# Kernel tuning notes

Measured on AMD Instinct MI355X. Metric: run time of the kernel, lower is better.

The kernel has to match this reference:

```python
import jax, jax.numpy as jnp
import numpy as np
from jax import lax

DIM = 4096
N_HEADS = 32
N_KV_HEADS = 8
HEAD_DIM = DIM // N_HEADS  # 128
N_REP = N_HEADS // N_KV_HEADS  # 4
B, S = 1, 2048
ROPE_THETA = 10000.0
NEG_INF = -1e9


def setup_inputs() -> dict:
    key = jax.random.key(0)
    ks = jax.random.split(key, 6)
    scale = 1.0 / np.sqrt(DIM)
    x = jax.random.normal(ks[0], (B, S, DIM), dtype=jnp.float32)
    wq = jax.random.normal(ks[1], (DIM, DIM), dtype=jnp.float32) * scale
    wk = jax.random.normal(ks[2], (N_KV_HEADS * HEAD_DIM, DIM), dtype=jnp.float32) * scale
    wv = jax.random.normal(ks[3], (N_KV_HEADS * HEAD_DIM, DIM), dtype=jnp.float32) * scale
    wo = jax.random.normal(ks[4], (DIM, DIM), dtype=jnp.float32) * scale
    # Llama rotary frequencies: freqs_cis[t, i] = exp(i * t * theta^(-2i/d))
    inv_freq = 1.0 / (ROPE_THETA ** (np.arange(0, HEAD_DIM, 2, dtype=np.float32) / HEAD_DIM))
    angles = np.outer(np.arange(S, dtype=np.float32), inv_freq)  # [S, HEAD_DIM//2]
    freqs_cos = jnp.asarray(np.cos(angles), dtype=jnp.float32)
    freqs_sin = jnp.asarray(np.sin(angles), dtype=jnp.float32)
    cache_k = jnp.zeros((B, S, N_KV_HEADS, HEAD_DIM), dtype=jnp.float32)
    cache_v = jnp.zeros((B, S, N_KV_HEADS, HEAD_DIM), dtype=jnp.float32)
    # causal mask added to scores (broadcasts over [B, H, S, S])
    mask = jnp.where(np.triu(np.ones((S, S), dtype=bool), k=1), NEG_INF, 0.0).astype(jnp.float32)
    return {"x": x, "wq": wq, "wk": wk, "wv": wv, "wo": wo,
            "freqs_cos": freqs_cos, "freqs_sin": freqs_sin,
            "cache_k": cache_k, "cache_v": cache_v, "mask": mask,
            "start_pos": 0}


def _apply_rotary(t, cos, sin):
    # t: [B, S, H, HEAD_DIM]; cos/sin: [S, HEAD_DIM//2]
    b, s, h, d = t.shape
    tr = t.reshape(b, s, h, d // 2, 2)
    a, bb = tr[..., 0], tr[..., 1]  # real / imag of consecutive pairs
    c = cos[None, :, None, :]
    sn = sin[None, :, None, :]
    out_r = a * c - bb * sn
    out_i = a * sn + bb * c
    return jnp.stack([out_r, out_i], axis=-1).reshape(b, s, h, d)


def reference(x, wq, wk, wv, wo, freqs_cos, freqs_sin, cache_k, cache_v, mask, start_pos):
    bsz, seqlen, _ = x.shape
    xq = jnp.einsum('bsd,od->bso', x, wq).reshape(bsz, seqlen, N_HEADS, HEAD_DIM)
    xk = jnp.einsum('bsd,od->bso', x, wk).reshape(bsz, seqlen, N_KV_HEADS, HEAD_DIM)
    xv = jnp.einsum('bsd,od->bso', x, wv).reshape(bsz, seqlen, N_KV_HEADS, HEAD_DIM)
    xq = _apply_rotary(xq, freqs_cos, freqs_sin)
    xk = _apply_rotary(xk, freqs_cos, freqs_sin)
    # KV-cache append
    cache_k = lax.dynamic_update_slice(cache_k, xk, (0, start_pos, 0, 0))
    cache_v = lax.dynamic_update_slice(cache_v, xv, (0, start_pos, 0, 0))
    kv_len = start_pos + seqlen
    keys = cache_k[:, :kv_len]    # [B, KVLEN, KV, HD]
    values = cache_v[:, :kv_len]
    # GQA: repeat_interleave over kv heads
    keys = jnp.repeat(keys, N_REP, axis=2)      # [B, KVLEN, H, HD]
    values = jnp.repeat(values, N_REP, axis=2)
    q = xq.transpose(0, 2, 1, 3)       # [B, H, S, HD]
    k = keys.transpose(0, 2, 1, 3)     # [B, H, KVLEN, HD]
    v = values.transpose(0, 2, 1, 3)
    scores = jnp.einsum('bhqd,bhkd->bhqk', q, k) / np.sqrt(HEAD_DIM)
    scores = scores + mask[None, None, :, :]
    probs = jax.nn.softmax(scores.astype(jnp.float32), axis=-1).astype(q.dtype)
    out = jnp.einsum('bhqk,bhkd->bhqd', probs, v)
    out = out.transpose(0, 2, 1, 3).reshape(bsz, seqlen, -1)
    return jnp.einsum('bso,do->bsd', out, wo)
```

## Files before the change

### kernel.cpp

```cpp
#include <hip/hip_runtime.h>
#include <hip/hip_bf16.h>

typedef unsigned short u16;
typedef unsigned int u32;
typedef __bf16 bf16x8 __attribute__((ext_vector_type(8)));
typedef float f32x4 __attribute__((ext_vector_type(4)));
typedef u32 u32x4 __attribute__((ext_vector_type(4)));

#define QKV_LD 6144
#define KOFF 4096
#define VOFF 5120
#define HD 128
#define DIM 4096

__device__ __forceinline__ u16 f2bf(float f) {
  union { __hip_bfloat16 h; u16 u; } c;
  c.h = __float2bfloat16(f);
  return c.u;
}
__device__ __forceinline__ float bf2f(u16 u) {
  union { u16 u; __hip_bfloat16 h; } c;
  c.u = u;
  return __bfloat162float(c.h);
}

typedef __attribute__((address_space(1))) const u32 gas_u32;
typedef __attribute__((address_space(3))) u32 las_u32;
__device__ __forceinline__ void async16(const u16* g, u16* l) {
  __builtin_amdgcn_global_load_lds((gas_u32*)g, (las_u32*)l, 16, 0, 0);
}

__device__ __forceinline__ void store_out(u16* p, float v) { *p = f2bf(v); }
__device__ __forceinline__ void store_out(float* p, float v) { *p = v; }

__global__ __launch_bounds__(256) void cvt_kernel(const float* __restrict__ src,
                                                  u16* __restrict__ dst, int n8) {
  int i = blockIdx.x * 256 + threadIdx.x;
  if (i >= n8) return;
  const f32x4* s4 = (const f32x4*)src;
  f32x4 a = s4[2 * i], b = s4[2 * i + 1];
  u32x4 o;
  o[0] = (u32)f2bf(a[0]) | ((u32)f2bf(a[1]) << 16);
  o[1] = (u32)f2bf(a[2]) | ((u32)f2bf(a[3]) << 16);
  o[2] = (u32)f2bf(b[0]) | ((u32)f2bf(b[1]) << 16);
  o[3] = (u32)f2bf(b[2]) | ((u32)f2bf(b[3]) << 16);
  ((u32x4*)dst)[i] = o;
}

template <typename OutT>
__global__ __launch_bounds__(256, 2) void gemm_nt(const u16* __restrict__ A,
                                                  const u16* __restrict__ B,
                                                  OutT* __restrict__ C, int N, int K) {
  __shared__ u16 As[128 * 32];
  __shared__ u16 Bs[128 * 32];
  const int tid = threadIdx.x;
  const int wave = tid >> 6;
  const int lane = tid & 63;
  const int quad = lane >> 4;
  const int l16 = lane & 15;
  const int bm = blockIdx.y;
  const int bn = blockIdx.x;
  const int wm = (wave >> 1) * 64;
  const int wn = (wave & 1) * 64;

  f32x4 acc[4][4];
#pragma unroll
  for (int i = 0; i < 4; ++i)
#pragma unroll
    for (int j = 0; j < 4; ++j) {
      f32x4 z = {0.f, 0.f, 0.f, 0.f};
      acc[i][j] = z;
    }

  const int srow0 = wave * 32 + (lane >> 2);
  const int scol = (((lane & 3) ^ ((lane >> 2) & 3)) * 8);
  u16* ldsA0 = &As[(wave * 2 + 0) * 512];
  u16* ldsA1 = &As[(wave * 2 + 1) * 512];
  u16* ldsB0 = &Bs[(wave * 2 + 0) * 512];
  u16* ldsB1 = &Bs[(wave * 2 + 1) * 512];
  const u16* Ag0 = A + (size_t)(bm * 128 + srow0) * K + scol;
  const u16* Ag1 = A + (size_t)(bm * 128 + srow0 + 16) * K + scol;
  const u16* Bg0 = B + (size_t)(bn * 128 + srow0) * K + scol;
  const u16* Bg1 = B + (size_t)(bn * 128 + srow0 + 16) * K + scol;

  int aoff[4], boff[4];
#pragma unroll
  for (int mi = 0; mi < 4; ++mi)
    aoff[mi] = (wm + mi * 16 + l16) * 32 + ((quad ^ (l16 & 3)) * 8);
#pragma unroll
  for (int ni = 0; ni < 4; ++ni)
    boff[ni] = (wn + ni * 16 + l16) * 32 + ((quad ^ (l16 & 3)) * 8);

  for (int k0 = 0; k0 < K; k0 += 32) {
    __syncthreads();
    async16(Ag0 + k0, ldsA0);
    async16(Ag1 + k0, ldsA1);
    async16(Bg0 + k0, ldsB0);
    async16(Bg1 + k0, ldsB1);
    __syncthreads();
    bf16x8 af[4], bb[4];
#pragma unroll
    for (int mi = 0; mi < 4; ++mi) af[mi] = *(const bf16x8*)&As[aoff[mi]];
#pragma unroll
    for (int ni = 0; ni < 4; ++ni) bb[ni] = *(const bf16x8*)&Bs[boff[ni]];
#pragma unroll
    for (int mi = 0; mi < 4; ++mi)
#pragma unroll
      for (int ni = 0; ni < 4; ++ni)
        acc[mi][ni] = __builtin_amdgcn_mfma_f32_16x16x32_bf16(af[mi], bb[ni], acc[mi][ni], 0, 0, 0);
  }

#pragma unroll
  for (int mi = 0; mi < 4; ++mi) {
    int row = bm * 128 + wm + mi * 16 + quad * 4;
#pragma unroll
    for (int ni = 0; ni < 4; ++ni) {
      int col = bn * 128 + wn + ni * 16 + l16;
#pragma unroll
      for (int r = 0; r < 4; ++r)
        store_out(&C[(size_t)(row + r) * N + col], acc[mi][ni][r]);
    }
  }
}

#define BAR8 __builtin_amdgcn_s_barrier()
#define LGKM0                                                     \
  do {                                                            \
    asm volatile("s_waitcnt lgkmcnt(0)" ::: "memory");            \
    __builtin_amdgcn_sched_barrier(0);                            \
  } while (0)
#define VMC(n)                                                    \
  do {                                                            \
    asm volatile("s_waitcnt vmcnt(" #n ")" ::: "memory");         \
    __builtin_amdgcn_sched_barrier(0);                            \
  } while (0)

#define LDA8(buf, half, arr)                                                     \
  _Pragma("unroll") for (int mi = 0; mi < 4; ++mi) {                             \
    const int r_ = wm * 64 + mi * 16 + l16;                                      \
    const u16* p_ = &lds[buf][half][r_ * 64];                                    \
    _Pragma("unroll") for (int ks = 0; ks < 2; ++ks)                             \
      arr[mi][ks] = *(const bf16x8*)(p_ + (((ks * 4 + quad) ^ (r_ & 7)) << 3));  \
  }

#define LDB8(buf, half, arr)                                                     \
  _Pragma("unroll") for (int ni = 0; ni < 2; ++ni) {                             \
    const int r_ = wn * 32 + ni * 16 + l16;                                      \
    const u16* p_ = &lds[buf][2 + (half)][r_ * 64];                              \
    _Pragma("unroll") for (int ks = 0; ks < 2; ++ks)                             \
      arr[ni][ks] = *(const bf16x8*)(p_ + (((ks * 4 + quad) ^ (r_ & 7)) << 3));  \
  }

#define MMA8(qm, qn, af, bf)                                                       \
  __builtin_amdgcn_s_setprio(1);                                                   \
  _Pragma("unroll") for (int mi = 0; mi < 4; ++mi)                                 \
  _Pragma("unroll") for (int ni = 0; ni < 2; ++ni)                                 \
  _Pragma("unroll") for (int ks = 0; ks < 2; ++ks)                                 \
    acc[(qm) * 4 + mi][(qn) * 2 + ni] = __builtin_amdgcn_mfma_f32_16x16x32_bf16(   \
        af[mi][ks], bf[ni][ks], acc[(qm) * 4 + mi][(qn) * 2 + ni], 0, 0, 0);       \
  __builtin_amdgcn_s_setprio(0);

template <typename OutT>
__global__ __launch_bounds__(512, 2) void gemm_nt8(const u16* __restrict__ A,
                                                   const u16* __restrict__ B,
                                                   OutT* __restrict__ C,
                                                   int N, int K, int MT) {
  __shared__ u16 lds[2][4][128 * 64];
  const int tid = threadIdx.x;
  const int wave = tid >> 6;
  const int lane = tid & 63;
  const int quad = lane >> 4;
  const int l16 = lane & 15;
  const int wm = wave >> 2;
  const int wn = wave & 3;

  const int nwg = gridDim.x;
  const int bid = blockIdx.x;
  const int qq = nwg >> 3, rr8 = nwg & 7, xcd = bid & 7, off = bid >> 3;
  const int wg = (xcd < rr8 ? xcd * (qq + 1) : rr8 * (qq + 1) + (xcd - rr8) * qq) + off;
  const int bm = wg % MT;
  const int bn = wg / MT;

  const int NIT = K >> 7;

  const int srow = (wave << 3) + (lane >> 3);
  const int sgran = (lane & 7) ^ ((lane >> 3) & 7);
  const u16* Abase = A + (size_t)(bm * 256 + srow) * K + sgran * 8;
  const u16* Bbase = B + (size_t)(bn * 256 + srow) * K + sgran * 8;

  auto stage = [&](const u16* base, int h, int kt, u16* slot) {
    const u16* g = base + (size_t)(h * 128) * K + kt * 64;
    u16* s = slot + wave * (8 * 64);
    async16(g, s);
    async16(g + (size_t)64 * K, s + 64 * 64);
  };

  f32x4 acc[8][4];
#pragma unroll
  for (int i = 0; i < 8; ++i)
#pragma unroll
    for (int j = 0; j < 4; ++j) {
      f32x4 z = {0.f, 0.f, 0.f, 0.f};
      acc[i][j] = z;
    }

  stage(Abase, 0, 0, &lds[0][0][0]);
  stage(Bbase, 0, 0, &lds[0][2][0]);
  stage(Bbase, 1, 0, &lds[0][3][0]);
  stage(Abase, 1, 0, &lds[0][1][0]);
  stage(Abase, 0, 1, &lds[1][0][0]);
  stage(Bbase, 0, 1, &lds[1][2][0]);
  stage(Bbase, 1, 1, &lds[1][3][0]);
  VMC(6);
  BAR8;

  bf16x8 a0[4][2], a1[4][2], b0[2][2], b1[2][2];
  for (int it = 0; it < NIT; ++it) {
    const int t2 = 2 * it + 2, t3 = 2 * it + 3;
    const bool more = (it + 1 < NIT);

    LDA8(0, 0, a0);
    LDB8(0, 0, b0);
    stage(Abase, 1, 2 * it + 1, &lds[1][1][0]);
    BAR8; LGKM0;
    MMA8(0, 0, a0, b0);
    BAR8;
    LDB8(0, 1, b1);
    if (more) stage(Abase, 0, t2, &lds[0][0][0]);
    BAR8; LGKM0;
    MMA8(0, 1, a0, b1);
    BAR8;
    LDA8(0, 1, a1);
    if (more) stage(Bbase, 0, t2, &lds[0][2][0]);
    BAR8; LGKM0;
    MMA8(1, 1, a1, b1);
    BAR8;
    if (more) stage(Bbase, 1, t2, &lds[0][3][0]);
    BAR8; LGKM0;
    MMA8(1, 0, a1, b0);
    if (more) { VMC(6); } else { VMC(0); }
    BAR8;
    LDA8(1, 0, a0);
    LDB8(1, 0, b0);
    if (more) stage(Abase, 1, t2, &lds[0][1][0]);
    BAR8; LGKM0;
    MMA8(0, 0, a0, b0);
    BAR8;
    LDB8(1, 1, b1);
    if (more) stage(Abase, 0, t3, &lds[1][0][0]);
    BAR8; LGKM0;
    MMA8(0, 1, a0, b1);
    BAR8;
    LDA8(1, 1, a1);
    if (more) stage(Bbase, 0, t3, &lds[1][2][0]);
    BAR8; LGKM0;
    MMA8(1, 1, a1, b1);
    BAR8;
    if (more) stage(Bbase, 1, t3, &lds[1][3][0]);
    BAR8; LGKM0;
    MMA8(1, 0, a1, b0);
    if (more) { VMC(6); } else { VMC(0); }
    BAR8;
  }

#pragma unroll
  for (int qm = 0; qm < 2; ++qm)
#pragma unroll
    for (int mi = 0; mi < 4; ++mi) {
      int row = bm * 256 + qm * 128 + wm * 64 + mi * 16 + quad * 4;
#pragma unroll
      for (int qn = 0; qn < 2; ++qn)
#pragma unroll
        for (int ni = 0; ni < 2; ++ni) {
          int col = bn * 256 + qn * 128 + wn * 32 + ni * 16 + l16;
#pragma unroll
          for (int r = 0; r < 4; ++r)
            store_out(&C[(size_t)(row + r) * N + col], acc[qm * 4 + mi][qn * 2 + ni][r]);
        }
    }
}

__global__ __launch_bounds__(256) void rope_kernel(u16* qkv, const float* __restrict__ fcos,
                                                   const float* __restrict__ fsin) {
  int idx = blockIdx.x * 256 + threadIdx.x;
  int row, colbase, fi;
  if (idx < 2048 * 2048) {
    row = idx >> 11;
    int pi = idx & 2047;
    fi = pi & 63;
    colbase = (pi >> 6) * 128 + fi * 2;
  } else {
    int j = idx - 2048 * 2048;
    row = j >> 9;
    int pj = j & 511;
    fi = pj & 63;
    colbase = KOFF + (pj >> 6) * 128 + fi * 2;
  }
  float c = fcos[row * 64 + fi], s = fsin[row * 64 + fi];
  u32* p = (u32*)(qkv + (size_t)row * QKV_LD + colbase);
  u32 v = *p;
  float a = bf2f((u16)(v & 0xffffu));
  float b = bf2f((u16)(v >> 16));
  float xr = a * c - b * s;
  float xi = a * s + b * c;
  *p = (u32)f2bf(xr) | ((u32)f2bf(xi) << 16);
}

__global__ __launch_bounds__(256) void vtrans_kernel(const u16* __restrict__ qkv,
                                                     u16* __restrict__ vt) {
  __shared__ u16 Ls[64 * 72];
  const int tid = threadIdx.x;
  const int st = blockIdx.x, dt = blockIdx.y, kvh = blockIdx.z;
#pragma unroll
  for (int t = 0; t < 2; ++t) {
    int g = t * 256 + tid;
    int s = g >> 3, c = g & 7;
    u32x4 v = *(const u32x4*)(qkv + (size_t)(st * 64 + s) * QKV_LD + VOFF + kvh * HD + dt * 64 + c * 8);
    *(u32x4*)&Ls[s * 72 + c * 8] = v;
  }
  __syncthreads();
#pragma unroll
  for (int t = 0; t < 2; ++t) {
    int g = t * 256 + tid;
    int d = g >> 3, c2 = g & 7;
    u32x4 o;
#pragma unroll
    for (int j = 0; j < 4; ++j) {
      u16 lo = Ls[(c2 * 8 + 2 * j) * 72 + d];
      u16 hi = Ls[(c2 * 8 + 2 * j + 1) * 72 + d];
      o[j] = (u32)lo | ((u32)hi << 16);
    }
    *(u32x4*)(vt + (size_t)(kvh * HD + dt * 64 + d) * 2048 + st * 64 + c2 * 8) = o;
  }
}

__global__ __launch_bounds__(256, 2) void flash_kernel(const u16* __restrict__ qkv,
                                                       const u16* __restrict__ vt,
                                                       u16* __restrict__ attnb) {
  __shared__ u16 Kl[2][64 * 128];
  __shared__ u16 VtL[2][128 * 64];
  __shared__ u16 Pl[4][16 * 72];
  const int tid = threadIdx.x;
  const int wave = tid >> 6;
  const int lane = tid & 63;
  const int quad = lane >> 4;
  const int l16 = lane & 15;
  const int lid = blockIdx.x;
  const int h = lid & 31;
  const int z = lid >> 5;
  const int qt = (z < 8) ? z : 23 - z;
  const int kvh = h >> 2;
  const float scale = 0.08838834764831845f;
  const int nkt = 2 * qt + 2;

  const int krow_l = (lane >> 4);
  const int kcol_l = (lane & 15);
  const int vd_l = (lane >> 3);
  const int vc = (lane & 7) ^ ((lane >> 3) & 7);

  const u16* kbase = qkv + (size_t)KOFF + kvh * HD;
  const u16* vbase = vt + (size_t)kvh * HD * 2048;

  bf16x8 qf[2][4];
#pragma unroll
  for (int mi = 0; mi < 2; ++mi) {
    const u16* qp = qkv + (size_t)(qt * 128 + wave * 32 + mi * 16 + l16) * QKV_LD + h * HD + quad * 8;
#pragma unroll
    for (int ks = 0; ks < 4; ++ks) qf[mi][ks] = *(const bf16x8*)(qp + ks * 32);
  }

  f32x4 o[2][8];
#pragma unroll
  for (int mi = 0; mi < 2; ++mi)
#pragma unroll
    for (int i = 0; i < 8; ++i) { f32x4 zz = {0.f, 0.f, 0.f, 0.f}; o[mi][i] = zz; }
  float lacc[2] = {0.f, 0.f};

#pragma unroll
  for (int t = 0; t < 4; ++t) {
    int i = wave * 4 + t;
    int row = i * 4 + krow_l;
    int c = kcol_l ^ (row & 15);
    async16(kbase + (size_t)row * QKV_LD + c * 8, &Kl[0][i * 512]);
  }
#pragma unroll
  for (int t = 0; t < 4; ++t) {
    int i = wave * 4 + t;
    int d = i * 8 + vd_l;
    async16(vbase + (size_t)d * 2048 + vc * 8, &VtL[0][i * 512]);
  }

  for (int kt = 0; kt < nkt; ++kt) {
    const int cur = kt & 1;
    __syncthreads();

    f32x4 s4[2][4];
#pragma unroll
    for (int mi = 0; mi < 2; ++mi)
#pragma unroll
      for (int nb = 0; nb < 4; ++nb) { f32x4 zz = {0.f, 0.f, 0.f, 0.f}; s4[mi][nb] = zz; }
#pragma unroll
    for (int nb = 0; nb < 4; ++nb) {
#pragma unroll
      for (int ks = 0; ks < 4; ++ks) {
        int rr = nb * 16 + l16;
        int cc = ((ks * 4 + quad) ^ l16) * 8;
        bf16x8 kf = *(const bf16x8*)&Kl[cur][rr * 128 + cc];
        s4[0][nb] = __builtin_amdgcn_mfma_f32_16x16x32_bf16(qf[0][ks], kf, s4[0][nb], 0, 0, 0);
        s4[1][nb] = __builtin_amdgcn_mfma_f32_16x16x32_bf16(qf[1][ks], kf, s4[1][nb], 0, 0, 0);
      }
    }

    bf16x8 vb[16];
#pragma unroll
    for (int db = 0; db < 8; ++db) {
      int dd = db * 16 + l16;
#pragma unroll
      for (int ks2 = 0; ks2 < 2; ++ks2) {
        int c = (ks2 * 4 + quad) ^ (dd & 7);
        vb[db * 2 + ks2] = *(const bf16x8*)&VtL[cur][dd * 64 + c * 8];
      }
    }

    float p[2][4][4];
    const bool diag = (kt >= 2 * qt);
    if (diag) {
#pragma unroll
      for (int mi = 0; mi < 2; ++mi)
#pragma unroll
        for (int nb = 0; nb < 4; ++nb) {
          int col = kt * 64 + nb * 16 + l16;
#pragma unroll
          for (int r = 0; r < 4; ++r) {
            int row = qt * 128 + wave * 32 + mi * 16 + quad * 4 + r;
            p[mi][nb][r] = (col > row) ? 0.f : __expf(s4[mi][nb][r] * scale);
          }
        }
    } else {
#pragma unroll
      for (int mi = 0; mi < 2; ++mi)
#pragma unroll
        for (int nb = 0; nb < 4; ++nb)
#pragma unroll
          for (int r = 0; r < 4; ++r)
            p[mi][nb][r] = __expf(s4[mi][nb][r] * scale);
    }

    bf16x8 pa[2][2];
#pragma unroll
    for (int mi = 0; mi < 2; ++mi) {
#pragma unroll
      for (int nb = 0; nb < 4; ++nb)
#pragma unroll
        for (int r = 0; r < 4; ++r)
          Pl[wave][(quad * 4 + r) * 72 + nb * 16 + l16] = f2bf(p[mi][nb][r]);
      __asm__ __volatile__("s_waitcnt lgkmcnt(0)" ::: "memory");
#pragma unroll
      for (int ks2 = 0; ks2 < 2; ++ks2)
        pa[mi][ks2] = *(const bf16x8*)&Pl[wave][l16 * 72 + ks2 * 32 + quad * 8];
    }

#pragma unroll
    for (int mi = 0; mi < 2; ++mi) {
      float sm = 0.f;
#pragma unroll
      for (int ks2 = 0; ks2 < 2; ++ks2)
#pragma unroll
        for (int j = 0; j < 8; ++j) sm += (float)pa[mi][ks2][j];
      sm += __shfl_xor(sm, 16);
      sm += __shfl_xor(sm, 32);
      lacc[mi] += sm;
    }

    if (kt + 1 < nkt) {
      const u16* kb = kbase + (size_t)(kt + 1) * 64 * QKV_LD;
      const u16* vb2 = vbase + (kt + 1) * 64;
#pragma unroll
      for (int t = 0; t < 4; ++t) {
        int i = wave * 4 + t;
        int row = i * 4 + krow_l;
        int c = kcol_l ^ (row & 15);
        async16(kb + (size_t)row * QKV_LD + c * 8, &Kl[1 - cur][i * 512]);
      }
#pragma unroll
      for (int t = 0; t < 4; ++t) {
        int i = wave * 4 + t;
        int d = i * 8 + vd_l;
        async16(vb2 + (size_t)d * 2048 + vc * 8, &VtL[1 - cur][i * 512]);
      }
    }

#pragma unroll
    for (int mi = 0; mi < 2; ++mi)
#pragma unroll
      for (int db = 0; db < 8; ++db)
#pragma unroll
        for (int ks2 = 0; ks2 < 2; ++ks2)
          o[mi][db] = __builtin_amdgcn_mfma_f32_16x16x32_bf16(pa[mi][ks2], vb[db * 2 + ks2], o[mi][db], 0, 0, 0);
  }

  float* lsh = (float*)&Pl[wave][0];
  if (quad == 0) {
    lsh[l16] = lacc[0];
    lsh[16 + l16] = lacc[1];
  }
  __asm__ __volatile__("s_waitcnt lgkmcnt(0)" ::: "memory");
  __builtin_amdgcn_wave_barrier();
  f32x4 inv[2];
#pragma unroll
  for (int mi = 0; mi < 2; ++mi) {
    f32x4 lv = *(const f32x4*)&lsh[mi * 16 + quad * 4];
#pragma unroll
    for (int r = 0; r < 4; ++r) inv[mi][r] = 1.f / lv[r];
  }
#pragma unroll
  for (int mi = 0; mi < 2; ++mi)
#pragma unroll
    for (int db = 0; db < 8; ++db)
#pragma unroll
      for (int r = 0; r < 4; ++r) {
        int row = qt * 128 + wave * 32 + mi * 16 + quad * 4 + r;
        int col = h * HD + db * 16 + l16;
        attnb[(size_t)row * DIM + col] = f2bf(o[mi][db][r] * inv[mi][r]);
      }
}

extern "C" void kernel_launch(void* const* d_in, const int* in_sizes, int n_in,
                              void* d_out, int out_size, void* d_ws, size_t ws_size,
                              hipStream_t stream) {
  (void)in_sizes; (void)n_in; (void)out_size; (void)ws_size;
  const float* x    = (const float*)d_in[0];
  const float* wq   = (const float*)d_in[1];
  const float* wk   = (const float*)d_in[2];
  const float* wv   = (const float*)d_in[3];
  const float* wo   = (const float*)d_in[4];
  const float* fcos = (const float*)d_in[5];
  const float* fsin = (const float*)d_in[6];
  float* out = (float*)d_out;

  char* ws = (char*)d_ws;
  u16* xb    = (u16*)(ws);
  u16* wqkvb = (u16*)(ws + (size_t)16777216);
  u16* wob   = (u16*)(ws + (size_t)67108864);
  u16* qkv   = (u16*)(ws + (size_t)100663296);
  u16* attnb = (u16*)(ws + (size_t)125829120);
  u16* vtb   = (u16*)(ws);

  cvt_kernel<<<4096, 256, 0, stream>>>(x, xb, 1048576);
  cvt_kernel<<<8192, 256, 0, stream>>>(wq, wqkvb, 2097152);
  cvt_kernel<<<2048, 256, 0, stream>>>(wk, wqkvb + 16777216, 524288);
  cvt_kernel<<<2048, 256, 0, stream>>>(wv, wqkvb + 20971520, 524288);
  cvt_kernel<<<8192, 256, 0, stream>>>(wo, wob, 2097152);

  gemm_nt8<u16><<<dim3(192), 512, 0, stream>>>(xb, wqkvb, qkv, 6144, 4096, 8);
  vtrans_kernel<<<dim3(32, 2, 8), 256, 0, stream>>>(qkv, vtb);
  rope_kernel<<<20480, 256, 0, stream>>>(qkv, fcos, fsin);
  flash_kernel<<<512, 256, 0, stream>>>(qkv, vtb, attnb);
  gemm_nt<float><<<dim3(32, 16), 256, 0, stream>>>(attnb, wob, out, 4096, 4096);
}
```

Measured before the change: 550.5 us.

## Replace output projection GEMM with pipelined 128x256 8-wave kernel

The output projection, previously a simple 128x128 tile GEMM with two barriers per 32-wide K step, now runs on a new 512-thread kernel. It uses 128x256 tiles, double-buffered 64-wide K staging with async loads interleaved between MFMA phases, and XCD-aware block remapping over 256 workgroups. The goal is to hide global load latency and make better use of the MFMA units for the 4096x4096x2048 GEMM. The wait macros also lose their sched_barrier, which gives the compiler more scheduling freedom but could reorder code around the waits, and this applies to the existing gemm_nt8 as well.

After: 535.2 us. 1.03x faster.

```diff
diff --git a/kernel.cpp b/kernel.cpp
--- a/kernel.cpp
+++ b/kernel.cpp
@@ -47,93 +47,9 @@
   ((u32x4*)dst)[i] = o;
 }
 
-template <typename OutT>
-__global__ __launch_bounds__(256, 2) void gemm_nt(const u16* __restrict__ A,
-                                                  const u16* __restrict__ B,
-                                                  OutT* __restrict__ C, int N, int K) {
-  __shared__ u16 As[128 * 32];
-  __shared__ u16 Bs[128 * 32];
-  const int tid = threadIdx.x;
-  const int wave = tid >> 6;
-  const int lane = tid & 63;
-  const int quad = lane >> 4;
-  const int l16 = lane & 15;
-  const int bm = blockIdx.y;
-  const int bn = blockIdx.x;
-  const int wm = (wave >> 1) * 64;
-  const int wn = (wave & 1) * 64;
-
-  f32x4 acc[4][4];
-#pragma unroll
-  for (int i = 0; i < 4; ++i)
-#pragma unroll
-    for (int j = 0; j < 4; ++j) {
-      f32x4 z = {0.f, 0.f, 0.f, 0.f};
-      acc[i][j] = z;
-    }
-
-  const int srow0 = wave * 32 + (lane >> 2);
-  const int scol = (((lane & 3) ^ ((lane >> 2) & 3)) * 8);
-  u16* ldsA0 = &As[(wave * 2 + 0) * 512];
-  u16* ldsA1 = &As[(wave * 2 + 1) * 512];
-  u16* ldsB0 = &Bs[(wave * 2 + 0) * 512];
-  u16* ldsB1 = &Bs[(wave * 2 + 1) * 512];
-  const u16* Ag0 = A + (size_t)(bm * 128 + srow0) * K + scol;
-  const u16* Ag1 = A + (size_t)(bm * 128 + srow0 + 16) * K + scol;
-  const u16* Bg0 = B + (size_t)(bn * 128 + srow0) * K + scol;
-  const u16* Bg1 = B + (size_t)(bn * 128 + srow0 + 16) * K + scol;
-
-  int aoff[4], boff[4];
-#pragma unroll
-  for (int mi = 0; mi < 4; ++mi)
-    aoff[mi] = (wm + mi * 16 + l16) * 32 + ((quad ^ (l16 & 3)) * 8);
-#pragma unroll
-  for (int ni = 0; ni < 4; ++ni)
-    boff[ni] = (wn + ni * 16 + l16) * 32 + ((quad ^ (l16 & 3)) * 8);
-
-  for (int k0 = 0; k0 < K; k0 += 32) {
-    __syncthreads();
-    async16(Ag0 + k0, ldsA0);
-    async16(Ag1 + k0, ldsA1);
-    async16(Bg0 + k0, ldsB0);
-    async16(Bg1 + k0, ldsB1);
-    __syncthreads();
-    bf16x8 af[4], bb[4];
-#pragma unroll
-    for (int mi = 0; mi < 4; ++mi) af[mi] = *(const bf16x8*)&As[aoff[mi]];
-#pragma unroll
-    for (int ni = 0; ni < 4; ++ni) bb[ni] = *(const bf16x8*)&Bs[boff[ni]];
-#pragma unroll
-    for (int mi = 0; mi < 4; ++mi)
-#pragma unroll
-      for (int ni = 0; ni < 4; ++ni)
-        acc[mi][ni] = __builtin_amdgcn_mfma_f32_16x16x32_bf16(af[mi], bb[ni], acc[mi][ni], 0, 0, 0);
-  }
-
-#pragma unroll
-  for (int mi = 0; mi < 4; ++mi) {
-    int row = bm * 128 + wm + mi * 16 + quad * 4;
-#pragma unroll
-    for (int ni = 0; ni < 4; ++ni) {
-      int col = bn * 128 + wn + ni * 16 + l16;
-#pragma unroll
-      for (int r = 0; r < 4; ++r)
-        store_out(&C[(size_t)(row + r) * N + col], acc[mi][ni][r]);
-    }
-  }
-}
-
 #define BAR8 __builtin_amdgcn_s_barrier()
-#define LGKM0                                                     \
-  do {                                                            \
-    asm volatile("s_waitcnt lgkmcnt(0)" ::: "memory");            \
-    __builtin_amdgcn_sched_barrier(0);                            \
-  } while (0)
-#define VMC(n)                                                    \
-  do {                                                            \
-    asm volatile("s_waitcnt vmcnt(" #n ")" ::: "memory");         \
-    __builtin_amdgcn_sched_barrier(0);                            \
-  } while (0)
+#define LGKM0 asm volatile("s_waitcnt lgkmcnt(0)" ::: "memory")
+#define VMC(n) asm volatile("s_waitcnt vmcnt(" #n ")" ::: "memory")
 
 #define LDA8(buf, half, arr)                                                     \
   _Pragma("unroll") for (int mi = 0; mi < 4; ++mi) {                             \
@@ -276,6 +192,149 @@
 #pragma unroll
           for (int r = 0; r < 4; ++r)
             store_out(&C[(size_t)(row + r) * N + col], acc[qm * 4 + mi][qn * 2 + ni][r]);
+        }
+    }
+}
+
+#define LDAW(buf, arr)                                                               \
+  _Pragma("unroll") for (int qm_ = 0; qm_ < 2; ++qm_)                                \
+  _Pragma("unroll") for (int mi = 0; mi < 2; ++mi) {                                 \
+    const int r_ = qm_ * 64 + wm * 32 + mi * 16 + l16;                               \
+    const u16* p_ = &lds[buf][0][r_ * 64];                                           \
+    _Pragma("unroll") for (int ks = 0; ks < 2; ++ks)                                 \
+      arr[qm_][mi][ks] = *(const bf16x8*)(p_ + (((ks * 4 + quad) ^ (r_ & 7)) << 3)); \
+  }
+
+#define LDBW(buf, h, arr)                                                        \
+  _Pragma("unroll") for (int ni = 0; ni < 2; ++ni) {                             \
+    const int r_ = wn * 32 + ni * 16 + l16;                                      \
+    const u16* p_ = &lds[buf][1 + (h)][r_ * 64];                                 \
+    _Pragma("unroll") for (int ks = 0; ks < 2; ++ks)                             \
+      arr[ni][ks] = *(const bf16x8*)(p_ + (((ks * 4 + quad) ^ (r_ & 7)) << 3));  \
+  }
+
+#define MMAW(qm, qn, af, bf)                                                       \
+  __builtin_amdgcn_s_setprio(1);                                                   \
+  _Pragma("unroll") for (int mi = 0; mi < 2; ++mi)                                 \
+  _Pragma("unroll") for (int ni = 0; ni < 2; ++ni)                                 \
+  _Pragma("unroll") for (int ks = 0; ks < 2; ++ks)                                 \
+    acc[(qm) * 2 + mi][(qn) * 2 + ni] = __builtin_amdgcn_mfma_f32_16x16x32_bf16(   \
+        af[qm][mi][ks], bf[ni][ks], acc[(qm) * 2 + mi][(qn) * 2 + ni], 0, 0, 0);   \
+  __builtin_amdgcn_s_setprio(0);
+
+template <typename OutT>
+__global__ __launch_bounds__(512, 2) void gemm_nt8w(const u16* __restrict__ A,
+                                                    const u16* __restrict__ B,
+                                                    OutT* __restrict__ C,
+                                                    int N, int K, int MT) {
+  __shared__ u16 lds[2][3][128 * 64];
+  const int tid = threadIdx.x;
+  const int wave = tid >> 6;
+  const int lane = tid & 63;
+  const int quad = lane >> 4;
+  const int l16 = lane & 15;
+  const int wm = wave >> 2;
+  const int wn = wave & 3;
+
+  const int nwg = gridDim.x;
+  const int bid = blockIdx.x;
+  const int qq = nwg >> 3, rr8 = nwg & 7, xcd = bid & 7, off = bid >> 3;
+  const int wg = (xcd < rr8 ? xcd * (qq + 1) : rr8 * (qq + 1) + (xcd - rr8) * qq) + off;
+  const int bm = wg % MT;
+  const int bn = wg / MT;
+
+  const int NIT = K >> 7;
+
+  const int srow = (wave << 3) + (lane >> 3);
+  const int sgran = (lane & 7) ^ ((lane >> 3) & 7);
+  const u16* Abase = A + (size_t)(bm * 128 + srow) * K + sgran * 8;
+  const u16* Bbase = B + (size_t)(bn * 256 + srow) * K + sgran * 8;
+
+  auto stageA = [&](int buf, int kt) {
+    const u16* g = Abase + (size_t)kt * 64;
+    u16* s = &lds[buf][0][0] + wave * (8 * 64);
+    async16(g, s);
+    async16(g + (size_t)64 * K, s + 64 * 64);
+  };
+  auto stageB = [&](int buf, int h, int kt) {
+    const u16* g = Bbase + (size_t)(h * 128) * K + kt * 64;
+    u16* s = &lds[buf][1 + h][0] + wave * (8 * 64);
+    async16(g, s);
+    async16(g + (size_t)64 * K, s + 64 * 64);
+  };
+
+  f32x4 acc[4][4];
+#pragma unroll
+  for (int i = 0; i < 4; ++i)
+#pragma unroll
+    for (int j = 0; j < 4; ++j) {
+      f32x4 z = {0.f, 0.f, 0.f, 0.f};
+      acc[i][j] = z;
+    }
+
+  stageA(0, 0); stageB(0, 0, 0); stageB(0, 1, 0);
+  stageA(1, 1); stageB(1, 0, 1); stageB(1, 1, 1);
+  VMC(6);
+  BAR8;
+
+  bf16x8 a[2][2][2], b0f[2][2], b1f[2][2];
+  for (int it = 0; it < NIT; ++it) {
+    const int t2 = 2 * it + 2, t3 = 2 * it + 3;
+    const bool more = (it + 1 < NIT);
+
+    LDAW(0, a);
+    LDBW(0, 0, b0f);
+    BAR8; LGKM0;
+    MMAW(0, 0, a, b0f);
+    BAR8;
+    LDBW(0, 1, b1f);
+    if (more) stageB(0, 0, t2);
+    BAR8; LGKM0;
+    MMAW(0, 1, a, b1f);
+    BAR8;
+    if (more) stageA(0, t2);
+    BAR8; LGKM0;
+    MMAW(1, 1, a, b1f);
+    BAR8;
+    if (more) stageB(0, 1, t2);
+    BAR8; LGKM0;
+    MMAW(1, 0, a, b0f);
+    if (more) { VMC(6); } else { VMC(0); }
+    BAR8;
+    LDAW(1, a);
+    LDBW(1, 0, b0f);
+    BAR8; LGKM0;
+    MMAW(0, 0, a, b0f);
+    BAR8;
+    LDBW(1, 1, b1f);
+    if (more) stageB(1, 0, t3);
+    BAR8; LGKM0;
+    MMAW(0, 1, a, b1f);
+    BAR8;
+    if (more) stageA(1, t3);
+    BAR8; LGKM0;
+    MMAW(1, 1, a, b1f);
+    BAR8;
+    if (more) stageB(1, 1, t3);
+    BAR8; LGKM0;
+    MMAW(1, 0, a, b0f);
+    if (more) { VMC(6); } else { VMC(0); }
+    BAR8;
+  }
+
+#pragma unroll
+  for (int qm = 0; qm < 2; ++qm)
+#pragma unroll
+    for (int mi = 0; mi < 2; ++mi) {
+      int row = bm * 128 + qm * 64 + wm * 32 + mi * 16 + quad * 4;
+#pragma unroll
+      for (int qn = 0; qn < 2; ++qn)
+#pragma unroll
+        for (int ni = 0; ni < 2; ++ni) {
+          int col = bn * 256 + qn * 128 + wn * 32 + ni * 16 + l16;
+#pragma unroll
+          for (int r = 0; r < 4; ++r)
+            store_out(&C[(size_t)(row + r) * N + col], acc[qm * 2 + mi][qn * 2 + ni][r]);
         }
     }
 }
@@ -556,5 +615,5 @@
   vtrans_kernel<<<dim3(32, 2, 8), 256, 0, stream>>>(qkv, vtb);
   rope_kernel<<<20480, 256, 0, stream>>>(qkv, fcos, fsin);
   flash_kernel<<<512, 256, 0, stream>>>(qkv, vtb, attnb);
-  gemm_nt<float><<<dim3(32, 16), 256, 0, stream>>>(attnb, wob, out, 4096, 4096);
-}
+  gemm_nt8w<float><<<dim3(256), 512, 0, stream>>>(attnb, wob, out, 4096, 4096, 16);
+}
```
